# Optimization experiments

Measured on AMD Instinct MI355X. Metric: run time of the kernel, lower is better.

## Reference

```python
import jax, jax.numpy as jnp
import numpy as np

N = 100000
E = 6400000
H = 32  # num_hidden


def setup_inputs() -> dict:
    key = jax.random.key(0)
    ks = jax.random.split(key, 10)
    x = jax.random.normal(ks[0], (N,), dtype=jnp.float32)
    u = jax.random.normal(ks[1], (N,), dtype=jnp.float32)
    edge_index = jax.random.randint(ks[2], (2, E), 0, N, dtype=jnp.int64)
    # MLP(2 -> H -> H -> 1), 3 linear layers with relu between
    def lin(k, fan_in, fan_out):
        bound = 1.0 / np.sqrt(fan_in)
        kw, kb = jax.random.split(k)
        W = jax.random.uniform(kw, (fan_in, fan_out), jnp.float32, -bound, bound)
        b = jax.random.uniform(kb, (fan_out,), jnp.float32, -bound, bound)
        return W, b
    W1, b1 = lin(ks[3], 2, H)
    W2, b2 = lin(ks[4], H, H)
    W3, b3 = lin(ks[5], H, 1)
    return {"x": x, "edge_index": edge_index, "u": u,
            "W1": W1, "b1": b1, "W2": W2, "b2": b2, "W3": W3, "b3": b3}


def reference(x, edge_index, u, W1, b1, W2, b2, W3, b3):
    src, dst = edge_index[0], edge_index[1]
    # gather node scalars, form per-edge feature [E, 2]
    x_edge = jnp.stack([x[src], x[dst]], axis=-1)
    # per-edge MLP: 2 -> H -> H -> 1 with relu
    h = jax.nn.relu(x_edge @ W1 + b1)
    h = jax.nn.relu(h @ W2 + b2)
    w = (h @ W3 + b3)[:, 0]  # [E]
    # spmm: f[i] = sum_{e: src[e]=i} w[e] * u[dst[e]]
    f = jax.ops.segment_sum(w * u[dst], src, num_segments=x.shape[0])
    return f
```

## Files before the change

kernel.cpp:

```cpp
#include <hip/hip_runtime.h>

#define H 32
#define NSEG 2000
#define RBITS 9
#define RANGE 512
#define SPLIT 8
#define SEGPER (NSEG / SPLIT)
#define MAXROWS 260
#define EBMAX 3200

typedef __attribute__((ext_vector_type(2))) __fp16 half2v;
typedef __attribute__((ext_vector_type(8))) __fp16 half8;
typedef __attribute__((ext_vector_type(4))) float f32x4;
typedef unsigned int u32;
typedef unsigned short u16;

union HU { int i[4]; half8 h; };

static __device__ __forceinline__ int pkrtz(float a, float b) {
    return __builtin_bit_cast(int, __builtin_amdgcn_cvt_pkrtz(a, b));
}

static __device__ __forceinline__ float fdot2f(int w, int ab, float c) {
    return __builtin_amdgcn_fdot2(__builtin_bit_cast(half2v, w),
                                  __builtin_bit_cast(half2v, ab), c, false);
}

struct Invar {
    int   w1p[8];
    float b1v[8];
    half8 afrag[2];
    f32x4 c0, c1;
    float w3lo[4], w3hi[4];
    float b3v;
};

static __device__ __forceinline__ void load_invar(
    Invar& v, int g, int col,
    const float* __restrict__ W1, const float* __restrict__ b1,
    const float* __restrict__ W2, const float* __restrict__ b2,
    const float* __restrict__ W3, const float* __restrict__ b3)
{
    const int klo = 4 * g, khi = 16 + 4 * g;
#pragma unroll
    for (int i = 0; i < 4; ++i) {
        v.w1p[i]     = pkrtz(W1[klo + i], W1[H + klo + i]);
        v.w1p[4 + i] = pkrtz(W1[khi + i], W1[H + khi + i]);
        v.b1v[i]     = b1[klo + i];
        v.b1v[4 + i] = b1[khi + i];
    }
#pragma unroll
    for (int mt = 0; mt < 2; ++mt) {
        HU ua;
        const int c = mt * 16 + col;
        ua.i[0] = pkrtz(W2[(klo + 0) * H + c], W2[(klo + 1) * H + c]);
        ua.i[1] = pkrtz(W2[(klo + 2) * H + c], W2[(klo + 3) * H + c]);
        ua.i[2] = pkrtz(W2[(khi + 0) * H + c], W2[(khi + 1) * H + c]);
        ua.i[3] = pkrtz(W2[(khi + 2) * H + c], W2[(khi + 3) * H + c]);
        v.afrag[mt] = ua.h;
    }
#pragma unroll
    for (int r = 0; r < 4; ++r) {
        v.c0[r] = b2[klo + r]; v.c1[r] = b2[khi + r];
        v.w3lo[r] = W3[klo + r]; v.w3hi[r] = W3[khi + r];
    }
    v.b3v = b3[0];
}

static __device__ __forceinline__ float edge_w(const Invar& v, int g, int col, int abpk)
{
    float wred0 = 0.f, wred1 = 0.f, wred2 = 0.f, wred3 = 0.f;
#pragma unroll
    for (int T = 0; T < 4; ++T) {
        const int abT = __builtin_amdgcn_ds_bpermute(((T << 4) + col) << 2, abpk);
        const float h0 = fmaxf(fdot2f(v.w1p[0], abT, v.b1v[0]), 0.f);
        const float h1 = fmaxf(fdot2f(v.w1p[1], abT, v.b1v[1]), 0.f);
        const float h2 = fmaxf(fdot2f(v.w1p[2], abT, v.b1v[2]), 0.f);
        const float h3 = fmaxf(fdot2f(v.w1p[3], abT, v.b1v[3]), 0.f);
        const float h4 = fmaxf(fdot2f(v.w1p[4], abT, v.b1v[4]), 0.f);
        const float h5 = fmaxf(fdot2f(v.w1p[5], abT, v.b1v[5]), 0.f);
        const float h6 = fmaxf(fdot2f(v.w1p[6], abT, v.b1v[6]), 0.f);
        const float h7 = fmaxf(fdot2f(v.w1p[7], abT, v.b1v[7]), 0.f);

        HU ub;
        ub.i[0] = pkrtz(h0, h1);
        ub.i[1] = pkrtz(h2, h3);
        ub.i[2] = pkrtz(h4, h5);
        ub.i[3] = pkrtz(h6, h7);

        f32x4 acc0 = __builtin_amdgcn_mfma_f32_16x16x32_f16(v.afrag[0], ub.h, v.c0, 0, 0, 0);
        f32x4 acc1 = __builtin_amdgcn_mfma_f32_16x16x32_f16(v.afrag[1], ub.h, v.c1, 0, 0, 0);

        float p = 0.f;
#pragma unroll
        for (int r = 0; r < 4; ++r) {
            p += fmaxf(acc0[r], 0.f) * v.w3lo[r];
            p += fmaxf(acc1[r], 0.f) * v.w3hi[r];
        }
        p += __shfl_xor(p, 16, 64);
        p += __shfl_xor(p, 32, 64);
        const float wt = p + v.b3v;
        if      (T == 0) wred0 = wt;
        else if (T == 1) wred1 = wt;
        else if (T == 2) wred2 = wt;
        else             wred3 = wt;
    }
    const float wa = (g & 1) ? wred1 : wred0;
    const float wb = (g & 1) ? wred3 : wred2;
    return (g & 2) ? wb : wa;
}

__global__ void xu_pack_kernel(const float* __restrict__ x, const float* __restrict__ u,
                               float2* __restrict__ xu, int n) {
    int i = blockIdx.x * 256 + threadIdx.x;
    if (i < n) xu[i] = make_float2(x[i], u[i]);
}

__global__ __launch_bounds__(256) void p1_kernel(
    const float* __restrict__ x,
    const int*   __restrict__ ei,
    const float2* __restrict__ xu,
    const float* __restrict__ W1, const float* __restrict__ b1,
    const float* __restrict__ W2, const float* __restrict__ b2,
    const float* __restrict__ W3, const float* __restrict__ b3,
    u32* __restrict__ pairs, u32* __restrict__ offs,
    int E, int Eb, int nbuk)
{
    __shared__ u32 cnt[MAXROWS];
    __shared__ u32 cur[MAXROWS];
    __shared__ u32 wsum[4];
    __shared__ u32 lds_pairs[EBMAX];
    const int tid  = threadIdx.x;
    const int lane = tid & 63;
    const int wv   = tid >> 6;
    const int g    = lane >> 4;
    const int col  = lane & 15;
    const int b    = blockIdx.x;

    const int slice0 = b * Eb;
    int sliceN = E - slice0;
    if (sliceN < 0) sliceN = 0;
    if (sliceN > Eb) sliceN = Eb;

    Invar v;
    load_invar(v, g, col, W1, b1, W2, b2, W3, b3);

    for (int k = tid; k <= nbuk; k += 256) cnt[k] = 0;
    __syncthreads();
    if (((slice0 & 3) == 0) && ((sliceN & 3) == 0)) {
        const uint4* e4 = (const uint4*)(ei + slice0);
        const int n4 = sliceN >> 2;
        for (int i = tid; i < n4; i += 256) {
            const uint4 s4 = e4[i];
            atomicAdd(&cnt[s4.x >> RBITS], 1u);
            atomicAdd(&cnt[s4.y >> RBITS], 1u);
            atomicAdd(&cnt[s4.z >> RBITS], 1u);
            atomicAdd(&cnt[s4.w >> RBITS], 1u);
        }
    } else {
        for (int i = tid; i < sliceN; i += 256)
            atomicAdd(&cnt[((u32)ei[slice0 + i]) >> RBITS], 1u);
    }
    __syncthreads();

    {
        const u32 myc = (tid < nbuk) ? cnt[tid] : 0;
        u32 val = myc;
#pragma unroll
        for (int d = 1; d < 64; d <<= 1) {
            const u32 t = __shfl_up(val, d, 64);
            if (lane >= d) val += t;
        }
        if (lane == 63) wsum[wv] = val;
        __syncthreads();
        u32 woff = 0;
#pragma unroll
        for (int w = 0; w < 4; ++w) if (w < wv) woff += wsum[w];
        val += woff;
        if (tid < nbuk) cur[tid] = val - myc;
        if (tid == 0)   cur[nbuk] = wsum[0] + wsum[1] + wsum[2] + wsum[3];
    }
    __syncthreads();
    for (int k = tid; k <= nbuk; k += 256) offs[(size_t)b * (nbuk + 1) + k] = cur[k];
    __syncthreads();

    const int nbfull = sliceN >> 6;
    const int nquad  = nbfull >> 2;
    for (int q = wv; q < nquad; q += 4) {
        const int e0 = slice0 + (q << 8) + lane;
        const int e1 = e0 + 64, e2 = e0 + 128, e3 = e0 + 192;
        const int src0 = ei[e0],     src1 = ei[e1],     src2 = ei[e2],     src3 = ei[e3];
        const int dst0 = ei[E + e0], dst1 = ei[E + e1], dst2 = ei[E + e2], dst3 = ei[E + e3];
        const float  x0  = x[src0],  x1  = x[src1],  x2  = x[src2],  x3  = x[src3];
        const float2 xd0 = xu[dst0], xd1 = xu[dst1], xd2 = xu[dst2], xd3 = xu[dst3];

        const float w0 = edge_w(v, g, col, pkrtz(x0, xd0.x));
        const float w1 = edge_w(v, g, col, pkrtz(x1, xd1.x));
        const float w2 = edge_w(v, g, col, pkrtz(x2, xd2.x));
        const float w3 = edge_w(v, g, col, pkrtz(x3, xd3.x));

        const u32 pos0 = atomicAdd(&cur[((u32)src0) >> RBITS], 1u);
        lds_pairs[pos0] = ((u32)(u16)pkrtz(w0 * xd0.y, 0.0f)) | (((u32)src0 & (RANGE - 1)) << 16);
        const u32 pos1 = atomicAdd(&cur[((u32)src1) >> RBITS], 1u);
        lds_pairs[pos1] = ((u32)(u16)pkrtz(w1 * xd1.y, 0.0f)) | (((u32)src1 & (RANGE - 1)) << 16);
        const u32 pos2 = atomicAdd(&cur[((u32)src2) >> RBITS], 1u);
        lds_pairs[pos2] = ((u32)(u16)pkrtz(w2 * xd2.y, 0.0f)) | (((u32)src2 & (RANGE - 1)) << 16);
        const u32 pos3 = atomicAdd(&cur[((u32)src3) >> RBITS], 1u);
        lds_pairs[pos3] = ((u32)(u16)pkrtz(w3 * xd3.y, 0.0f)) | (((u32)src3 & (RANGE - 1)) << 16);
    }
    const int nbany = (sliceN + 63) >> 6;
    for (int bi = (nquad << 2) + wv; bi < nbany; bi += 4) {
        const int loc = (bi << 6) + lane;
        const bool valid = loc < sliceN;
        const int eL = slice0 + (valid ? loc : 0);
        const int src = ei[eL];
        const int dst = ei[E + eL];
        const float2 xud = xu[dst];
        const int abpk = pkrtz(x[src], xud.x);
        const float we = edge_w(v, g, col, abpk);
        if (valid) {
            const int buk = ((u32)src) >> RBITS;
            const u32 pos = atomicAdd(&cur[buk], 1u);
            lds_pairs[pos] = ((u32)(u16)pkrtz(we * xud.y, 0.0f)) | (((u32)src & (RANGE - 1)) << 16);
        }
    }
    __syncthreads();

    const int n4 = sliceN >> 2;
    const uint4* lp4 = (const uint4*)lds_pairs;
    uint4* gp4 = (uint4*)(pairs + slice0);
    for (int i = tid; i < n4; i += 256) gp4[i] = lp4[i];
    for (int i = (n4 << 2) + tid; i < sliceN; i += 256) pairs[slice0 + i] = lds_pairs[i];
}

__global__ __launch_bounds__(256) void p2_kernel(
    const u32* __restrict__ pairs, const u32* __restrict__ offs,
    float* __restrict__ pf, int Eb, int nbuk)
{
    __shared__ float acc[RANGE];
    __shared__ u32 so_l[SEGPER];
    __shared__ u32 pre[SEGPER + 1];
    __shared__ u32 wsum[4];
    const int tid = threadIdx.x;
    const int lane = tid & 63;
    const int wv  = tid >> 6;
    const int buk = blockIdx.x / SPLIT;
    const int sp  = blockIdx.x % SPLIT;

    acc[tid] = 0.f;
    acc[tid + 256] = 0.f;
    u32 myc = 0, so = 0;
    if (tid < SEGPER) {
        const int s = sp + tid * SPLIT;
        const u32* o = offs + (size_t)s * (nbuk + 1) + buk;
        so = o[0];
        myc = o[1] - so;
    }
    {
        u32 val = myc;
#pragma unroll
        for (int d = 1; d < 64; d <<= 1) {
            const u32 t = __shfl_up(val, d, 64);
            if (lane >= d) val += t;
        }
        if (lane == 63) wsum[wv] = val;
        __syncthreads();
        u32 woff = 0;
#pragma unroll
        for (int w = 0; w < 4; ++w) if (w < wv) woff += wsum[w];
        val += woff;
        if (tid < SEGPER) { so_l[tid] = so; pre[tid + 1] = val; }
        if (tid == 0) pre[0] = 0;
    }
    __syncthreads();

    const int total = (int)pre[SEGPER];
    for (int base = tid << 1; base < total; base += 512) {
#pragma unroll
        for (int k = 0; k < 2; ++k) {
            const int i = base + k;
            if (i >= total) break;
            int lo = 0, hi = SEGPER;
            while (hi - lo > 1) {
                const int mid = (lo + hi) >> 1;
                if (pre[mid] <= (u32)i) lo = mid; else hi = mid;
            }
            const int s = sp + lo * SPLIT;
            const u32 p = pairs[(size_t)s * Eb + so_l[lo] + (u32)i - pre[lo]];
            const float val = (float)__builtin_bit_cast(_Float16, (u16)(p & 0xffffu));
            atomicAdd(&acc[p >> 16], val);
        }
    }
    __syncthreads();

    const size_t stride = (size_t)nbuk * RANGE;
    const int node0 = buk * RANGE;
    pf[(size_t)sp * stride + node0 + tid] = acc[tid];
    pf[(size_t)sp * stride + node0 + tid + 256] = acc[tid + 256];
}

__global__ void freduce_kernel(const float* __restrict__ pf, float* __restrict__ f,
                               int n, int stride) {
    const int i = blockIdx.x * 256 + threadIdx.x;
    if (i >= n) return;
    float s = 0.f;
#pragma unroll
    for (int r = 0; r < SPLIT; ++r) s += pf[(size_t)r * stride + i];
    f[i] = s;
}

__global__ void zero_kernel(float* __restrict__ p, int n) {
    int i = blockIdx.x * blockDim.x + threadIdx.x;
    if (i < n) p[i] = 0.0f;
}

__global__ __launch_bounds__(256) void fb_kernel(
    const float* __restrict__ x,
    const int*   __restrict__ ei,
    const float* __restrict__ u,
    const float* __restrict__ W1, const float* __restrict__ b1,
    const float* __restrict__ W2, const float* __restrict__ b2,
    const float* __restrict__ W3, const float* __restrict__ b3,
    float* __restrict__ f, int E)
{
    const int lane = threadIdx.x & 63;
    const int g    = lane >> 4;
    const int col  = lane & 15;

    Invar v;
    load_invar(v, g, col, W1, b1, W2, b2, W3, b3);

    const int nbatch = E >> 6;
    const int gw = blockIdx.x * 4 + (threadIdx.x >> 6);
    const int nw = gridDim.x * 4;
    for (int bt = gw; bt < nbatch; bt += nw) {
        const int e   = (bt << 6) + lane;
        const int src = ei[e];
        const int dst = ei[E + e];
        const int abpk = pkrtz(x[src], x[dst]);
        const float ud = u[dst];
        const float we = edge_w(v, g, col, abpk);
        atomicAdd(&f[src], we * ud);
    }
}

extern "C" void kernel_launch(void* const* d_in, const int* in_sizes, int n_in,
                              void* d_out, int out_size, void* d_ws, size_t ws_size,
                              hipStream_t stream) {
    const float* x  = (const float*)d_in[0];
    const int*   ei = (const int*)d_in[1];
    const float* u  = (const float*)d_in[2];
    const float* W1 = (const float*)d_in[3];
    const float* b1 = (const float*)d_in[4];
    const float* W2 = (const float*)d_in[5];
    const float* b2 = (const float*)d_in[6];
    const float* W3 = (const float*)d_in[7];
    const float* b3 = (const float*)d_in[8];
    float* f = (float*)d_out;

    const int n = in_sizes[0];
    const int E = in_sizes[1] / 2;

    const int nbuk = (n + RANGE - 1) / RANGE;
    const int Eb = (((E + NSEG - 1) / NSEG) + 63) & ~63;
    const size_t stride = (size_t)nbuk * RANGE;
    const size_t need = ((size_t)NSEG * Eb + (size_t)(nbuk + 1) * NSEG + (size_t)SPLIT * stride)
                        * sizeof(u32);
    const bool xu_fits = (size_t)SPLIT * stride * sizeof(float) >= (size_t)n * sizeof(float2);

    if (nbuk + 1 <= MAXROWS && nbuk <= 256 && Eb <= EBMAX && ws_size >= need
        && (E & 63) == 0 && xu_fits) {
        u32* pairs = (u32*)d_ws;
        u32* offs  = pairs + (size_t)NSEG * Eb;
        float* pf  = (float*)(offs + (size_t)(nbuk + 1) * NSEG);
        float2* xu = (float2*)pf;

        xu_pack_kernel<<<(n + 255) / 256, 256, 0, stream>>>(x, u, xu, n);
        p1_kernel<<<NSEG, 256, 0, stream>>>(x, ei, xu, W1, b1, W2, b2, W3, b3,
                                            pairs, offs, E, Eb, nbuk);
        p2_kernel<<<nbuk * SPLIT, 256, 0, stream>>>(pairs, offs, pf, Eb, nbuk);
        freduce_kernel<<<(n + 255) / 256, 256, 0, stream>>>(pf, f, n, (int)stride);
    } else {
        zero_kernel<<<(n + 255) / 256, 256, 0, stream>>>(f, n);
        fb_kernel<<<2048, 256, 0, stream>>>(x, ei, u, W1, b1, W2, b2, W3, b3, f, E);
    }
}
```

Before: 132.8 us.

## Compute first MLP layer with MFMA and halve segment count

Replaces the eight per-lane fdot2 instructions for the first 2->32 layer with two zero-padded 16x16x32 MFMAs, taking layer-1 work off the VALU and onto the matrix units. It also halves NSEG and SPLIT and doubles EBMAX, so each block handles more edges. The padded MFMAs use only a small part of their K dimension, so the matrix units do mostly wasted work. The larger segments change how work is parallelised and may raise LDS or register use.

```diff
diff --git a/kernel.cpp b/kernel.cpp
--- a/kernel.cpp
+++ b/kernel.cpp
@@ -1,13 +1,13 @@
 #include <hip/hip_runtime.h>
 
 #define H 32
-#define NSEG 2000
+#define NSEG 1000
 #define RBITS 9
 #define RANGE 512
-#define SPLIT 8
+#define SPLIT 4
 #define SEGPER (NSEG / SPLIT)
 #define MAXROWS 260
-#define EBMAX 3200
+#define EBMAX 6400
 
 typedef __attribute__((ext_vector_type(2))) __fp16 half2v;
 typedef __attribute__((ext_vector_type(8))) __fp16 half8;
@@ -21,14 +21,9 @@
     return __builtin_bit_cast(int, __builtin_amdgcn_cvt_pkrtz(a, b));
 }
 
-static __device__ __forceinline__ float fdot2f(int w, int ab, float c) {
-    return __builtin_amdgcn_fdot2(__builtin_bit_cast(half2v, w),
-                                  __builtin_bit_cast(half2v, ab), c, false);
-}
-
 struct Invar {
-    int   w1p[8];
-    float b1v[8];
+    half8 a1frag[2];
+    f32x4 c1a, c1b;
     half8 afrag[2];
     f32x4 c0, c1;
     float w3lo[4], w3hi[4];
@@ -43,11 +38,16 @@
 {
     const int klo = 4 * g, khi = 16 + 4 * g;
 #pragma unroll
-    for (int i = 0; i < 4; ++i) {
-        v.w1p[i]     = pkrtz(W1[klo + i], W1[H + klo + i]);
-        v.w1p[4 + i] = pkrtz(W1[khi + i], W1[H + khi + i]);
-        v.b1v[i]     = b1[klo + i];
-        v.b1v[4 + i] = b1[khi + i];
+    for (int mt = 0; mt < 2; ++mt) {
+        HU ua;
+        const int j = mt * 16 + col;
+        ua.i[0] = (g == 0) ? pkrtz(W1[j], W1[H + j]) : 0;
+        ua.i[1] = 0; ua.i[2] = 0; ua.i[3] = 0;
+        v.a1frag[mt] = ua.h;
+    }
+#pragma unroll
+    for (int r = 0; r < 4; ++r) {
+        v.c1a[r] = b1[klo + r]; v.c1b[r] = b1[khi + r];
     }
 #pragma unroll
     for (int mt = 0; mt < 2; ++mt) {
@@ -73,20 +73,18 @@
 #pragma unroll
     for (int T = 0; T < 4; ++T) {
         const int abT = __builtin_amdgcn_ds_bpermute(((T << 4) + col) << 2, abpk);
-        const float h0 = fmaxf(fdot2f(v.w1p[0], abT, v.b1v[0]), 0.f);
-        const float h1 = fmaxf(fdot2f(v.w1p[1], abT, v.b1v[1]), 0.f);
-        const float h2 = fmaxf(fdot2f(v.w1p[2], abT, v.b1v[2]), 0.f);
-        const float h3 = fmaxf(fdot2f(v.w1p[3], abT, v.b1v[3]), 0.f);
-        const float h4 = fmaxf(fdot2f(v.w1p[4], abT, v.b1v[4]), 0.f);
-        const float h5 = fmaxf(fdot2f(v.w1p[5], abT, v.b1v[5]), 0.f);
-        const float h6 = fmaxf(fdot2f(v.w1p[6], abT, v.b1v[6]), 0.f);
-        const float h7 = fmaxf(fdot2f(v.w1p[7], abT, v.b1v[7]), 0.f);
+
+        HU ub1;
+        ub1.i[0] = (g == 0) ? abT : 0;
+        ub1.i[1] = 0; ub1.i[2] = 0; ub1.i[3] = 0;
+        f32x4 d0 = __builtin_amdgcn_mfma_f32_16x16x32_f16(v.a1frag[0], ub1.h, v.c1a, 0, 0, 0);
+        f32x4 d1 = __builtin_amdgcn_mfma_f32_16x16x32_f16(v.a1frag[1], ub1.h, v.c1b, 0, 0, 0);
 
         HU ub;
-        ub.i[0] = pkrtz(h0, h1);
-        ub.i[1] = pkrtz(h2, h3);
-        ub.i[2] = pkrtz(h4, h5);
-        ub.i[3] = pkrtz(h6, h7);
+        ub.i[0] = pkrtz(fmaxf(d0[0], 0.f), fmaxf(d0[1], 0.f));
+        ub.i[1] = pkrtz(fmaxf(d0[2], 0.f), fmaxf(d0[3], 0.f));
+        ub.i[2] = pkrtz(fmaxf(d1[0], 0.f), fmaxf(d1[1], 0.f));
+        ub.i[3] = pkrtz(fmaxf(d1[2], 0.f), fmaxf(d1[3], 0.f));
 
         f32x4 acc0 = __builtin_amdgcn_mfma_f32_16x16x32_f16(v.afrag[0], ub.h, v.c0, 0, 0, 0);
         f32x4 acc1 = __builtin_amdgcn_mfma_f32_16x16x32_f16(v.afrag[1], ub.h, v.c1, 0, 0, 0);
```

Result: slower. 149.8 us (+12.8%).
